# Kernel tuning notes

Hardware: AMD Instinct MI355X
Metric: run time of the kernel (lower is better)

The kernel has to match this reference:

```python
import jax, jax.numpy as jnp
import numpy as np


def setup_inputs() -> dict:
    key = jax.random.key(0)
    k1, k2, k3 = jax.random.split(key, 3)
    N, M, D = 8192, 32768, 64
    source_data = jax.random.normal(k1, (N, D), dtype=jnp.float32)
    target_data = jax.random.normal(k2, (M, D), dtype=jnp.float32)
    psi = jax.random.normal(k3, (M,), dtype=jnp.float32)
    return {"source_data": source_data, "target_data": target_data, "psi": psi}


def reference(source_data, target_data, psi):
    # cost[n, m] = ||x_n||^2 + ||y_m||^2 - 2 <x_n, y_m>
    sq_src = jnp.sum(source_data ** 2, axis=1, keepdims=True)          # [N, 1]
    sq_tgt = jnp.sum(target_data ** 2, axis=1)[None, :]                # [1, M]
    cost = sq_src + sq_tgt - 2.0 * jnp.einsum('nd,md->nm', source_data, target_data)
    out = jnp.min(cost - psi[None, :], axis=1) + jnp.mean(psi)         # [N]
    return out
```

## Files before the change

### kernel.cpp

```cpp
#include <hip/hip_runtime.h>
#include <stdint.h>

typedef float  f32x4v __attribute__((ext_vector_type(4)));
typedef short  s16x8  __attribute__((ext_vector_type(8)));

constexpr int D      = 64;
constexpr int SPLITS = 64;
constexpr int CHM    = 512;
constexpr int G      = 16;

__device__ __forceinline__ unsigned short f2bf(float f) {
    unsigned int u = __float_as_uint(f);
    u = (u + 0x7FFFu + ((u >> 16) & 1u)) >> 16;
    return (unsigned short)u;
}

__device__ __forceinline__ void gload_lds16(const void* g, void* l) {
    __builtin_amdgcn_global_load_lds((__attribute__((address_space(1))) void*)g,
                                     (__attribute__((address_space(3))) void*)l, 16, 0, 0);
}
__device__ __forceinline__ void gload_lds4(const void* g, void* l) {
    __builtin_amdgcn_global_load_lds((__attribute__((address_space(1))) void*)g,
                                     (__attribute__((address_space(3))) void*)l, 4, 0, 0);
}

__global__ __launch_bounds__(256)
void prep(const float* __restrict__ X, const float* __restrict__ Y,
          const float* __restrict__ psi,
          unsigned short* __restrict__ Xb, unsigned short* __restrict__ Yb,
          float* __restrict__ t, float* __restrict__ sqx,
          float* __restrict__ psum_arr, int N, int M) {
    const int tid  = threadIdx.x;
    const int lane = tid & 63, wave = tid >> 6;
    const int r16  = lane & 15, q = lane >> 4;
    const int NYB = M >> 4, NXB = N >> 4;
    const int b = blockIdx.x;
    __shared__ float red[4];

    if (b < NYB) {
        const int row = b * 16 + wave * 4 + q;
        const float4 v = *reinterpret_cast<const float4*>(Y + (size_t)row * D + r16 * 4);
        uint2 p;
        p.x = (unsigned)f2bf(v.x) | ((unsigned)f2bf(v.y) << 16);
        p.y = (unsigned)f2bf(v.z) | ((unsigned)f2bf(v.w) << 16);
        *reinterpret_cast<uint2*>(Yb + (size_t)row * D + r16 * 4) = p;
        float s = v.x * v.x + v.y * v.y + v.z * v.z + v.w * v.w;
        #pragma unroll
        for (int off = 1; off <= 8; off <<= 1) s += __shfl_xor(s, off);
        if (r16 == 0) t[row] = s - psi[row];
    } else if (b < NYB + NXB) {
        const int row = (b - NYB) * 16 + wave * 4 + q;
        const float4 v = *reinterpret_cast<const float4*>(X + (size_t)row * D + r16 * 4);
        uint2 p;
        p.x = (unsigned)f2bf(-2.f * v.x) | ((unsigned)f2bf(-2.f * v.y) << 16);
        p.y = (unsigned)f2bf(-2.f * v.z) | ((unsigned)f2bf(-2.f * v.w) << 16);
        *reinterpret_cast<uint2*>(Xb + (size_t)row * D + r16 * 4) = p;
        float s = v.x * v.x + v.y * v.y + v.z * v.z + v.w * v.w;
        #pragma unroll
        for (int off = 1; off <= 8; off <<= 1) s += __shfl_xor(s, off);
        if (r16 == 0) sqx[row] = s;
    } else {
        const int g = b - NYB - NXB;
        float s = psi[g * 512 + tid] + psi[g * 512 + 256 + tid];
        #pragma unroll
        for (int off = 1; off <= 32; off <<= 1) s += __shfl_xor(s, off);
        if (lane == 0) red[wave] = s;
        __syncthreads();
        if (tid == 0) psum_arr[g] = red[0] + red[1] + red[2] + red[3];
    }
}

__global__ __launch_bounds__(256, 2)
void sdot_main(const unsigned short* __restrict__ Xb,
               const unsigned short* __restrict__ Yb,
               const float* __restrict__ t,
               float* __restrict__ partial, int M) {
    __shared__ __align__(16) unsigned short ly[CHM * D];
    __shared__ __align__(16) float lt[CHM];

    const int tid  = threadIdx.x;
    const int wave = tid >> 6, lane = tid & 63;
    const int quad = lane >> 4, r16 = lane & 15;
    const int chunk   = blockIdx.x;
    const int rowgrp  = blockIdx.y;
    const int m_begin = chunk * CHM;

    #pragma unroll
    for (int i = 0; i < 16; ++i) {
        const int idx = i * 256 + tid;
        const int row = idx >> 3, c = idx & 7;
        gload_lds16(Yb + (size_t)(m_begin + row) * D + ((c ^ (row & 7)) << 3),
                    &ly[(i * 256 + wave * 64) << 3]);
    }
    #pragma unroll
    for (int j = 0; j < 2; ++j)
        gload_lds4(t + m_begin + j * 256 + wave * 64 + lane, &lt[j * 256 + wave * 64]);

    s16x8 b[G][2];
    #pragma unroll
    for (int g = 0; g < G; ++g) {
        const int srow = rowgrp * (G * 64) + wave * (G * 16) + g * 16 + r16;
        #pragma unroll
        for (int h = 0; h < 2; ++h)
            b[g][h] = *reinterpret_cast<const s16x8*>(Xb + (size_t)srow * D + h * 32 + quad * 8);
    }

    float rmin[G];
    #pragma unroll
    for (int g = 0; g < G; ++g) rmin[g] = 1e30f;

    asm volatile("s_waitcnt vmcnt(0)" ::: "memory");
    __builtin_amdgcn_s_barrier();

    const int csw0 = (quad ^ (r16 & 7)) << 3;
    const int csw1 = ((quad + 4) ^ (r16 & 7)) << 3;
    #pragma unroll 4
    for (int st = 0; st < CHM / 16; ++st) {
        const int trow = st * 16 + r16;
        const s16x8 a0 = *reinterpret_cast<const s16x8*>(&ly[trow * D + csw0]);
        const s16x8 a1 = *reinterpret_cast<const s16x8*>(&ly[trow * D + csw1]);
        const f32x4v tv4 = *reinterpret_cast<const f32x4v*>(&lt[st * 16 + quad * 4]);

        f32x4v acc[G];
        __builtin_amdgcn_s_setprio(1);
        #pragma unroll
        for (int g = 0; g < G; ++g)
            acc[g] = __builtin_amdgcn_mfma_f32_16x16x32_bf16(a0, b[g][0], tv4, 0, 0, 0);
        #pragma unroll
        for (int g = 0; g < G; ++g)
            acc[g] = __builtin_amdgcn_mfma_f32_16x16x32_bf16(a1, b[g][1], acc[g], 0, 0, 0);
        __builtin_amdgcn_s_setprio(0);
        #pragma unroll
        for (int g = 0; g < G; ++g)
            rmin[g] = fminf(fminf(fminf(acc[g][0], acc[g][1]),
                                  fminf(acc[g][2], acc[g][3])), rmin[g]);
    }

    #pragma unroll
    for (int off = 16; off <= 32; off <<= 1)
        #pragma unroll
        for (int g = 0; g < G; ++g)
            rmin[g] = fminf(rmin[g], __shfl_xor(rmin[g], off));

    if (quad == 0) {
        #pragma unroll
        for (int g = 0; g < G; ++g) {
            const int row = rowgrp * (G * 64) + wave * (G * 16) + g * 16 + r16;
            partial[(size_t)row * SPLITS + chunk] = rmin[g];
        }
    }
}

__global__ __launch_bounds__(256)
void finalize(const float* __restrict__ sqx, const float* __restrict__ partial,
              const float* __restrict__ psum_arr, float* __restrict__ out, int M) {
    const int lane = threadIdx.x & 63, wave = threadIdx.x >> 6;
    const int row  = blockIdx.x * 4 + wave;
    float ps = psum_arr[lane];
    #pragma unroll
    for (int off = 1; off <= 32; off <<= 1) ps += __shfl_xor(ps, off);
    float pm = partial[(size_t)row * SPLITS + lane];
    #pragma unroll
    for (int off = 1; off <= 32; off <<= 1) pm = fminf(pm, __shfl_xor(pm, off));
    if (lane == 0) out[row] = sqx[row] + ps / (float)M + pm;
}

extern "C" void kernel_launch(void* const* d_in, const int* in_sizes, int n_in,
                              void* d_out, int out_size, void* d_ws, size_t ws_size,
                              hipStream_t stream) {
    const float* X   = (const float*)d_in[0];
    const float* Y   = (const float*)d_in[1];
    const float* psi = (const float*)d_in[2];
    float* out = (float*)d_out;

    const int N = in_sizes[0] / D;
    const int M = in_sizes[2];

    char* ws = (char*)d_ws;
    unsigned short* Yb = (unsigned short*)ws;
    size_t off = (size_t)M * D * sizeof(unsigned short);
    unsigned short* Xb = (unsigned short*)(ws + off);
    off += (size_t)N * D * sizeof(unsigned short);
    float* t = (float*)(ws + off);
    off += (size_t)M * sizeof(float);
    float* sqx = (float*)(ws + off);
    off += (size_t)N * sizeof(float);
    float* partial = (float*)(ws + off);
    off += (size_t)N * SPLITS * sizeof(float);
    float* psum_arr = (float*)(ws + off);

    prep<<<(M >> 4) + (N >> 4) + 64, 256, 0, stream>>>(X, Y, psi, Xb, Yb, t, sqx, psum_arr, N, M);
    sdot_main<<<dim3(SPLITS, N / (G * 64)), 256, 0, stream>>>(Xb, Yb, t, partial, M);
    finalize<<<N / 4, 256, 0, stream>>>(sqx, partial, psum_arr, out, M);
}
```

Measured before the change: 105.4 us.

## Use 512-thread blocks with fewer row groups per wave and software-prefetched A tiles

Each block now runs 8 waves of 8 row-groups instead of 4 waves of 16, so every block shares its 64KB LDS Y tile across twice as many waves and per-thread register use is halved. The t vector is read straight from global memory rather than staged in LDS. The main loop prefetches the next step's A fragments and t values before issuing the current MFMAs, and interleaves two independent MFMA chains with their min reductions. The intent is to raise occupancy and hide LDS latency, at the cost of more per-iteration global loads for t and the removal of the setprio hints.

```diff
diff --git a/kernel.cpp b/kernel.cpp
--- a/kernel.cpp
+++ b/kernel.cpp
@@ -7,7 +7,7 @@
 constexpr int D      = 64;
 constexpr int SPLITS = 64;
 constexpr int CHM    = 512;
-constexpr int G      = 16;
+constexpr int G      = 8;
 
 __device__ __forceinline__ unsigned short f2bf(float f) {
     unsigned int u = __float_as_uint(f);
@@ -18,10 +18,6 @@
 __device__ __forceinline__ void gload_lds16(const void* g, void* l) {
     __builtin_amdgcn_global_load_lds((__attribute__((address_space(1))) void*)g,
                                      (__attribute__((address_space(3))) void*)l, 16, 0, 0);
-}
-__device__ __forceinline__ void gload_lds4(const void* g, void* l) {
-    __builtin_amdgcn_global_load_lds((__attribute__((address_space(1))) void*)g,
-                                     (__attribute__((address_space(3))) void*)l, 4, 0, 0);
 }
 
 __global__ __launch_bounds__(256)
@@ -70,13 +66,12 @@
     }
 }
 
-__global__ __launch_bounds__(256, 2)
+__global__ __launch_bounds__(512, 4)
 void sdot_main(const unsigned short* __restrict__ Xb,
                const unsigned short* __restrict__ Yb,
                const float* __restrict__ t,
                float* __restrict__ partial, int M) {
     __shared__ __align__(16) unsigned short ly[CHM * D];
-    __shared__ __align__(16) float lt[CHM];
 
     const int tid  = threadIdx.x;
     const int wave = tid >> 6, lane = tid & 63;
@@ -86,20 +81,17 @@
     const int m_begin = chunk * CHM;
 
     #pragma unroll
-    for (int i = 0; i < 16; ++i) {
-        const int idx = i * 256 + tid;
+    for (int i = 0; i < 8; ++i) {
+        const int idx = i * 512 + tid;
         const int row = idx >> 3, c = idx & 7;
         gload_lds16(Yb + (size_t)(m_begin + row) * D + ((c ^ (row & 7)) << 3),
-                    &ly[(i * 256 + wave * 64) << 3]);
+                    &ly[(i * 512 + wave * 64) << 3]);
     }
-    #pragma unroll
-    for (int j = 0; j < 2; ++j)
-        gload_lds4(t + m_begin + j * 256 + wave * 64 + lane, &lt[j * 256 + wave * 64]);
 
     s16x8 b[G][2];
     #pragma unroll
     for (int g = 0; g < G; ++g) {
-        const int srow = rowgrp * (G * 64) + wave * (G * 16) + g * 16 + r16;
+        const int srow = rowgrp * 1024 + wave * (G * 16) + g * 16 + r16;
         #pragma unroll
         for (int h = 0; h < 2; ++h)
             b[g][h] = *reinterpret_cast<const s16x8*>(Xb + (size_t)srow * D + h * 32 + quad * 8);
@@ -114,26 +106,29 @@
 
     const int csw0 = (quad ^ (r16 & 7)) << 3;
     const int csw1 = ((quad + 4) ^ (r16 & 7)) << 3;
-    #pragma unroll 4
+    const float* tq = t + m_begin + quad * 4;
+
+    s16x8  a0 = *reinterpret_cast<const s16x8*>(&ly[r16 * D + csw0]);
+    s16x8  a1 = *reinterpret_cast<const s16x8*>(&ly[r16 * D + csw1]);
+    f32x4v tv = *reinterpret_cast<const f32x4v*>(tq);
+
     for (int st = 0; st < CHM / 16; ++st) {
-        const int trow = st * 16 + r16;
-        const s16x8 a0 = *reinterpret_cast<const s16x8*>(&ly[trow * D + csw0]);
-        const s16x8 a1 = *reinterpret_cast<const s16x8*>(&ly[trow * D + csw1]);
-        const f32x4v tv4 = *reinterpret_cast<const f32x4v*>(&lt[st * 16 + quad * 4]);
+        const int nst  = (st + 1) & (CHM / 16 - 1);
+        const int trow = nst * 16 + r16;
+        const s16x8  na0 = *reinterpret_cast<const s16x8*>(&ly[trow * D + csw0]);
+        const s16x8  na1 = *reinterpret_cast<const s16x8*>(&ly[trow * D + csw1]);
+        const f32x4v ntv = *reinterpret_cast<const f32x4v*>(tq + nst * 16);
 
-        f32x4v acc[G];
-        __builtin_amdgcn_s_setprio(1);
         #pragma unroll
-        for (int g = 0; g < G; ++g)
-            acc[g] = __builtin_amdgcn_mfma_f32_16x16x32_bf16(a0, b[g][0], tv4, 0, 0, 0);
-        #pragma unroll
-        for (int g = 0; g < G; ++g)
-            acc[g] = __builtin_amdgcn_mfma_f32_16x16x32_bf16(a1, b[g][1], acc[g], 0, 0, 0);
-        __builtin_amdgcn_s_setprio(0);
-        #pragma unroll
-        for (int g = 0; g < G; ++g)
-            rmin[g] = fminf(fminf(fminf(acc[g][0], acc[g][1]),
-                                  fminf(acc[g][2], acc[g][3])), rmin[g]);
+        for (int g = 0; g < G; g += 2) {
+            f32x4v p = __builtin_amdgcn_mfma_f32_16x16x32_bf16(a0, b[g    ][0], tv, 0, 0, 0);
+            f32x4v q = __builtin_amdgcn_mfma_f32_16x16x32_bf16(a0, b[g + 1][0], tv, 0, 0, 0);
+            p = __builtin_amdgcn_mfma_f32_16x16x32_bf16(a1, b[g    ][1], p, 0, 0, 0);
+            q = __builtin_amdgcn_mfma_f32_16x16x32_bf16(a1, b[g + 1][1], q, 0, 0, 0);
+            rmin[g]     = fminf(fminf(fminf(p[0], p[1]), fminf(p[2], p[3])), rmin[g]);
+            rmin[g + 1] = fminf(fminf(fminf(q[0], q[1]), fminf(q[2], q[3])), rmin[g + 1]);
+        }
+        a0 = na0; a1 = na1; tv = ntv;
     }
 
     #pragma unroll
@@ -145,7 +140,7 @@
     if (quad == 0) {
         #pragma unroll
         for (int g = 0; g < G; ++g) {
-            const int row = rowgrp * (G * 64) + wave * (G * 16) + g * 16 + r16;
+            const int row = rowgrp * 1024 + wave * (G * 16) + g * 16 + r16;
             partial[(size_t)row * SPLITS + chunk] = rmin[g];
         }
     }
@@ -190,6 +185,6 @@
     float* psum_arr = (float*)(ws + off);
 
     prep<<<(M >> 4) + (N >> 4) + 64, 256, 0, stream>>>(X, Y, psi, Xb, Yb, t, sqx, psum_arr, N, M);
-    sdot_main<<<dim3(SPLITS, N / (G * 64)), 256, 0, stream>>>(Xb, Yb, t, partial, M);
+    sdot_main<<<dim3(SPLITS, N / 1024), 512, 0, stream>>>(Xb, Yb, t, partial, M);
     finalize<<<N / 4, 256, 0, stream>>>(sqx, partial, psum_arr, out, M);
 }
```

New measurement: 106.2 us. Within noise of the previous version (+0.7%).

## Shrink sdot tiles for more blocks and software-pipeline MFMA with min fold

Applied to the files above, without the earlier changes.

The main kernel's work split is retiled: 128 M-splits of 256 targets each, and 4 row-groups per wave instead of 16. This cuts registers and LDS per block, so occupancy can rise to 4 blocks per CU and the grid grows to 4096 blocks. The step loop is manually double-buffered across two accumulator sets, so the min-fold of one step overlaps the MFMAs of the next. In exchange, each source tile now gets far less reuse of LDS-loaded target data, so LDS reads per MFMA and partial-result writes double, and finalize reads twice as many partials.

```diff
diff --git a/kernel.cpp b/kernel.cpp
--- a/kernel.cpp
+++ b/kernel.cpp
@@ -5,9 +5,10 @@
 typedef short  s16x8  __attribute__((ext_vector_type(8)));
 
 constexpr int D      = 64;
-constexpr int SPLITS = 64;
-constexpr int CHM    = 512;
-constexpr int G      = 16;
+constexpr int SPLITS = 128;
+constexpr int CHM    = 256;
+constexpr int G      = 4;
+constexpr int NT     = CHM / 16;
 
 __device__ __forceinline__ unsigned short f2bf(float f) {
     unsigned int u = __float_as_uint(f);
@@ -70,7 +71,7 @@
     }
 }
 
-__global__ __launch_bounds__(256, 2)
+__global__ __launch_bounds__(256, 4)
 void sdot_main(const unsigned short* __restrict__ Xb,
                const unsigned short* __restrict__ Yb,
                const float* __restrict__ t,
@@ -86,20 +87,18 @@
     const int m_begin = chunk * CHM;
 
     #pragma unroll
-    for (int i = 0; i < 16; ++i) {
+    for (int i = 0; i < 8; ++i) {
         const int idx = i * 256 + tid;
         const int row = idx >> 3, c = idx & 7;
         gload_lds16(Yb + (size_t)(m_begin + row) * D + ((c ^ (row & 7)) << 3),
                     &ly[(i * 256 + wave * 64) << 3]);
     }
-    #pragma unroll
-    for (int j = 0; j < 2; ++j)
-        gload_lds4(t + m_begin + j * 256 + wave * 64 + lane, &lt[j * 256 + wave * 64]);
+    gload_lds4(t + m_begin + wave * 64 + lane, &lt[wave * 64]);
 
     s16x8 b[G][2];
     #pragma unroll
     for (int g = 0; g < G; ++g) {
-        const int srow = rowgrp * (G * 64) + wave * (G * 16) + g * 16 + r16;
+        const int srow = rowgrp * 256 + wave * (G * 16) + g * 16 + r16;
         #pragma unroll
         for (int h = 0; h < 2; ++h)
             b[g][h] = *reinterpret_cast<const s16x8*>(Xb + (size_t)srow * D + h * 32 + quad * 8);
@@ -114,27 +113,39 @@
 
     const int csw0 = (quad ^ (r16 & 7)) << 3;
     const int csw1 = ((quad + 4) ^ (r16 & 7)) << 3;
-    #pragma unroll 4
-    for (int st = 0; st < CHM / 16; ++st) {
-        const int trow = st * 16 + r16;
-        const s16x8 a0 = *reinterpret_cast<const s16x8*>(&ly[trow * D + csw0]);
-        const s16x8 a1 = *reinterpret_cast<const s16x8*>(&ly[trow * D + csw1]);
-        const f32x4v tv4 = *reinterpret_cast<const f32x4v*>(&lt[st * 16 + quad * 4]);
-
-        f32x4v acc[G];
-        __builtin_amdgcn_s_setprio(1);
-        #pragma unroll
-        for (int g = 0; g < G; ++g)
-            acc[g] = __builtin_amdgcn_mfma_f32_16x16x32_bf16(a0, b[g][0], tv4, 0, 0, 0);
-        #pragma unroll
-        for (int g = 0; g < G; ++g)
-            acc[g] = __builtin_amdgcn_mfma_f32_16x16x32_bf16(a1, b[g][1], acc[g], 0, 0, 0);
-        __builtin_amdgcn_s_setprio(0);
-        #pragma unroll
-        for (int g = 0; g < G; ++g)
-            rmin[g] = fminf(fminf(fminf(acc[g][0], acc[g][1]),
-                                  fminf(acc[g][2], acc[g][3])), rmin[g]);
-    }
+
+#define SDOT_STEP(st, A_)                                                           \
+    {                                                                               \
+        const int trow = (st) * 16 + r16;                                           \
+        const s16x8 a0 = *reinterpret_cast<const s16x8*>(&ly[trow * D + csw0]);     \
+        const s16x8 a1 = *reinterpret_cast<const s16x8*>(&ly[trow * D + csw1]);     \
+        const f32x4v tv4 = *reinterpret_cast<const f32x4v*>(&lt[(st) * 16 + quad * 4]); \
+        __builtin_amdgcn_s_setprio(1);                                              \
+        _Pragma("unroll")                                                           \
+        for (int g = 0; g < G; ++g)                                                 \
+            A_[g] = __builtin_amdgcn_mfma_f32_16x16x32_bf16(a0, b[g][0], tv4, 0, 0, 0); \
+        _Pragma("unroll")                                                           \
+        for (int g = 0; g < G; ++g)                                                 \
+            A_[g] = __builtin_amdgcn_mfma_f32_16x16x32_bf16(a1, b[g][1], A_[g], 0, 0, 0); \
+        __builtin_amdgcn_s_setprio(0);                                              \
+    }
+#define SDOT_FOLD(A_)                                                               \
+    {                                                                               \
+        _Pragma("unroll")                                                           \
+        for (int g = 0; g < G; ++g)                                                 \
+            rmin[g] = fminf(fminf(fminf(A_[g][0], A_[g][1]),                        \
+                                  fminf(A_[g][2], A_[g][3])), rmin[g]);             \
+    }
+
+    f32x4v accA[G], accB[G];
+    SDOT_STEP(0, accB);
+    for (int p = 0; p < NT / 2 - 1; ++p) {
+        SDOT_STEP(2 * p + 1, accA);  SDOT_FOLD(accB);
+        SDOT_STEP(2 * p + 2, accB);  SDOT_FOLD(accA);
+    }
+    SDOT_STEP(NT - 1, accA);  SDOT_FOLD(accB);  SDOT_FOLD(accA);
+#undef SDOT_STEP
+#undef SDOT_FOLD
 
     #pragma unroll
     for (int off = 16; off <= 32; off <<= 1)
@@ -145,7 +156,7 @@
     if (quad == 0) {
         #pragma unroll
         for (int g = 0; g < G; ++g) {
-            const int row = rowgrp * (G * 64) + wave * (G * 16) + g * 16 + r16;
+            const int row = rowgrp * 256 + wave * (G * 16) + g * 16 + r16;
             partial[(size_t)row * SPLITS + chunk] = rmin[g];
         }
     }
@@ -159,7 +170,8 @@
     float ps = psum_arr[lane];
     #pragma unroll
     for (int off = 1; off <= 32; off <<= 1) ps += __shfl_xor(ps, off);
-    float pm = partial[(size_t)row * SPLITS + lane];
+    float pm = fminf(partial[(size_t)row * SPLITS + lane],
+                     partial[(size_t)row * SPLITS + 64 + lane]);
     #pragma unroll
     for (int off = 1; off <= 32; off <<= 1) pm = fminf(pm, __shfl_xor(pm, off));
     if (lane == 0) out[row] = sqx[row] + ps / (float)M + pm;
@@ -190,6 +202,6 @@
     float* psum_arr = (float*)(ws + off);
 
     prep<<<(M >> 4) + (N >> 4) + 64, 256, 0, stream>>>(X, Y, psi, Xb, Yb, t, sqx, psum_arr, N, M);
-    sdot_main<<<dim3(SPLITS, N / (G * 64)), 256, 0, stream>>>(Xb, Yb, t, partial, M);
+    sdot_main<<<dim3(SPLITS, N / 256), 256, 0, stream>>>(Xb, Yb, t, partial, M);
     finalize<<<N / 4, 256, 0, stream>>>(sqx, partial, psum_arr, out, M);
 }
```

After: 103.9 us. No clear change (-1.5%).
